# Performance work log

Hardware: AMD Instinct MI355X
Metric: run time of the kernel (lower is better)

The kernel has to match this reference:

```python
import jax, jax.numpy as jnp
import numpy as np

RADII = {1: 0.031, 2: 0.028, 3: 0.128, 4: 0.096, 5: 0.084, 6: 0.073, 7: 0.071, 8: 0.066, 9: 0.057, 10: 0.058, 11: 0.166, 12: 0.141, 13: 0.121, 14: 0.111, 15: 0.107, 16: 0.105, 17: 0.102, 18: 0.106, 19: 0.2029, 20: 0.176, 21: 0.17, 22: 0.16, 23: 0.153, 24: 0.139, 25: 0.15, 26: 0.142, 27: 0.138, 28: 0.124, 29: 0.132, 30: 0.122, 31: 0.122, 32: 0.12, 33: 0.119, 34: 0.12, 35: 0.12, 36: 0.116, 37: 0.22, 38: 0.195, 39: 0.19, 40: 0.175, 41: 0.164, 42: 0.154, 43: 0.147, 44: 0.146, 45: 0.142, 46: 0.139, 47: 0.145, 48: 0.144, 49: 0.142, 50: 0.139, 51: 0.139, 52: 0.138, 53: 0.139, 54: 0.14, 55: 0.244, 56: 0.215, 57: 0.207, 58: 0.204, 59: 0.2029, 60: 0.2009, 61: 0.199, 62: 0.198, 63: 0.198, 64: 0.196, 65: 0.194, 66: 0.192, 67: 0.192, 68: 0.189, 69: 0.19, 70: 0.187, 71: 0.187, 72: 0.175, 73: 0.17, 74: 0.162, 75: 0.151, 76: 0.144, 77: 0.141, 78: 0.136, 79: 0.136, 80: 0.132, 81: 0.145, 82: 0.146, 83: 0.148, 84: 0.14, 85: 0.15, 86: 0.15, 87: 0.26, 88: 0.221, 89: 0.215, 90: 0.206, 91: 0.2, 92: 0.196, 93: 0.19, 94: 0.187, 95: 0.18, 96: 0.169}

N_ATOMS = 1_000_000
N_EDGES = 16_000_000
NUM_SYSTEMS = 10_000
MAX_Z = 97  # atomic numbers 1..96 valid
COULOMB = 138.9354576   # kJ/mol * nm / e^2
A_PREF = 0.8854 * 0.0529177210903  # Bohr-radius prefactor in nm


def setup_inputs() -> dict:
    key = jax.random.key(0)
    k1, k2, k3, k4 = jax.random.split(key, 4)
    local_pair_indices = jax.random.randint(k1, (2, N_EDGES), 0, N_ATOMS)
    # positive distances in nm, safely away from zero
    local_d_ij = jax.random.uniform(k2, (N_EDGES,), jnp.float32, 0.01, 0.5)
    atomic_numbers = jax.random.randint(k3, (N_ATOMS,), 1, MAX_Z)
    atomic_subsystem_indices = jnp.sort(
        jax.random.randint(k4, (N_ATOMS,), 0, NUM_SYSTEMS))
    radii_table = np.zeros(MAX_Z, dtype=np.float32)
    for z, r in RADII.items():
        radii_table[z] = r
    return {
        'local_d_ij': local_d_ij,
        'radii_table': jnp.asarray(radii_table),
        'local_pair_indices': local_pair_indices,
        'atomic_numbers': atomic_numbers,
        'atomic_subsystem_indices': atomic_subsystem_indices,
    }


def reference(local_d_ij, radii_table, local_pair_indices, atomic_numbers,
              atomic_subsystem_indices):
    idx_i = local_pair_indices[0]
    idx_j = local_pair_indices[1]
    # torch filters edges by idx_i < idx_j (data-dependent shape); here we
    # keep fixed shapes and zero masked contributions -> identical sums.
    mask = idx_i < idx_j

    zi_int = atomic_numbers[idx_i]
    zj_int = atomic_numbers[idx_j]
    zi = zi_int.astype(jnp.float32)
    zj = zj_int.astype(jnp.float32)
    ri = radii_table[zi_int]
    rj = radii_table[zj_int]

    d_ij = local_d_ij
    a = A_PREF / (zi ** 0.23 + zj ** 0.23)
    d = d_ij / a
    f = (0.1818 * jnp.exp(-3.2 * d)
         + 0.5099 * jnp.exp(-0.9423 * d)
         + 0.2802 * jnp.exp(-0.4029 * d)
         + 0.02817 * jnp.exp(-0.2016 * d))
    rsum = ri + rj
    phi = jnp.where(d_ij < rsum,
                    0.5 * (jnp.cos(jnp.pi * d_ij / rsum) + 1.0),
                    0.0)
    energy = f * phi * COULOMB * zi * zj / d_ij
    energy = jnp.where(mask, energy, 0.0)

    seg = atomic_subsystem_indices[idx_i]
    per_system = jax.ops.segment_sum(energy, seg, num_segments=NUM_SYSTEMS)
    return per_system.reshape(-1, 1)
```

## Files before the change

### kernel.cpp

```cpp
#include <hip/hip_runtime.h>


constexpr int MAXZ = 97;
constexpr int NBINS_PAD = 10240;
constexpr int NREP = 512;
constexpr int NPART = 32;

constexpr double LOG2E_D = 1.4426950408889634;
constexpr float A_INV = (float)(1.0 / (0.8854 * 0.0529177210903));
constexpr float C1 = (float)(-3.2    * LOG2E_D);
constexpr float C2 = (float)(-0.9423 * LOG2E_D);
constexpr float C3 = (float)(-0.4029 * LOG2E_D);
constexpr float C4 = (float)(-0.2016 * LOG2E_D);
constexpr float COUL = 138.9354576f;

typedef int   iv4 __attribute__((ext_vector_type(4)));
typedef float fv4 __attribute__((ext_vector_type(4)));

__global__ void zero_kernel(float* __restrict__ out, int n) {
    int i = blockIdx.x * blockDim.x + threadIdx.x;
    if (i < n) out[i] = 0.0f;
}

__global__ void pack_kernel(const int* __restrict__ z,
                            const int* __restrict__ seg,
                            unsigned int* __restrict__ packed, int n) {
    int i = blockIdx.x * blockDim.x + threadIdx.x;
    if (i < n)
        packed[i] = (unsigned int)z[i] | ((unsigned int)seg[i] << 8);
}


__global__ __launch_bounds__(1024)
void zbl_hist_kernel(const float* __restrict__ d_ij,
                     const float* __restrict__ radii,
                     const int* __restrict__ idx_i,
                     const int* __restrict__ idx_j,
                     const unsigned int* __restrict__ packed,
                     float* __restrict__ rep,
                     int nchunk) {
    __shared__ float s_hist[NBINS_PAD];
    __shared__ float s_r[128];
    __shared__ float s_zp[128];
    const int t = threadIdx.x;

    for (int b = t; b < NBINS_PAD; b += 1024) s_hist[b] = 0.0f;
    if (t < 128) {
        s_r[t] = (t < MAXZ) ? radii[t] : 0.0f;
        s_zp[t] = __builtin_exp2f(0.23f * __builtin_log2f((float)t));
    }
    __syncthreads();

    const int stride = gridDim.x * blockDim.x;
    for (int c = blockIdx.x * blockDim.x + t; c < nchunk; c += stride) {
        iv4 ii = __builtin_nontemporal_load(
            reinterpret_cast<const iv4*>(idx_i) + c);
        iv4 jj = __builtin_nontemporal_load(
            reinterpret_cast<const iv4*>(idx_j) + c);
        fv4 dd = __builtin_nontemporal_load(
            reinterpret_cast<const fv4*>(d_ij) + c);

#pragma unroll
        for (int k = 0; k < 4; ++k) {
            int i = ii[k];
            int j = jj[k];
            float d = dd[k];
            if (i < j) {
                unsigned int pi = packed[i];
                unsigned int pj = packed[j];
                int zi = (int)(pi & 0xFFu);
                int zj = (int)(pj & 0xFFu);
                int seg = (int)(pi >> 8);
                float rsum = s_r[zi] + s_r[zj];
                if (d < rsum) {
                    float dA = d * (s_zp[zi] + s_zp[zj]) * A_INV;
                    float f = 0.1818f  * __builtin_exp2f(C1 * dA)
                            + 0.5099f  * __builtin_exp2f(C2 * dA)
                            + 0.2802f  * __builtin_exp2f(C3 * dA)
                            + 0.02817f * __builtin_exp2f(C4 * dA);
                    float tt = d * __builtin_amdgcn_rcpf(rsum);
                    float phi = 0.5f * (__builtin_amdgcn_cosf(0.5f * tt) + 1.0f);
                    float e = f * phi * (COUL * (float)zi * (float)zj)
                            * __builtin_amdgcn_rcpf(d);
                    atomicAdd(&s_hist[seg], e);
                }
            }
        }
    }

    __syncthreads();
    fv4* __restrict__ rp =
        reinterpret_cast<fv4*>(rep + (size_t)blockIdx.x * NBINS_PAD);
    const fv4* sh = reinterpret_cast<const fv4*>(s_hist);
    for (int q = t; q < NBINS_PAD / 4; q += 1024)
        __builtin_nontemporal_store(sh[q], rp + q);
}

__global__ __launch_bounds__(256)
void reduce1_kernel(const float* __restrict__ rep,
                    float* __restrict__ partial) {
    int bin = blockIdx.x * 256 + threadIdx.x;
    int s = blockIdx.y;
    float acc = 0.0f;
    for (int r = s; r < NREP; r += NPART)
        acc += rep[(size_t)r * NBINS_PAD + bin];
    partial[(size_t)s * NBINS_PAD + bin] = acc;
}

__global__ __launch_bounds__(256)
void reduce2_kernel(const float* __restrict__ partial,
                    float* __restrict__ out, int out_size) {
    int bin = blockIdx.x * 256 + threadIdx.x;
    if (bin < out_size) {
        float acc = 0.0f;
        for (int s = 0; s < NPART; ++s)
            acc += partial[(size_t)s * NBINS_PAD + bin];
        out[bin] = acc;
    }
}


template <bool PACKED>
__global__ __launch_bounds__(256)
void zbl_atomic_kernel(const float* __restrict__ d_ij,
                       const float* __restrict__ radii,
                       const int* __restrict__ idx_i,
                       const int* __restrict__ idx_j,
                       const unsigned int* __restrict__ packed,
                       const int* __restrict__ atomz,
                       const int* __restrict__ subsys,
                       float* __restrict__ out,
                       int nchunk) {
    __shared__ float s_r[128];
    __shared__ float s_zp[128];
    int t = threadIdx.x;
    if (t < 128) {
        s_r[t] = (t < MAXZ) ? radii[t] : 0.0f;
        s_zp[t] = __builtin_exp2f(0.23f * __builtin_log2f((float)t));
    }
    __syncthreads();

    int chunk = blockIdx.x * blockDim.x + threadIdx.x;
    if (chunk >= nchunk) return;

    iv4 ii = reinterpret_cast<const iv4*>(idx_i)[chunk];
    iv4 jj = reinterpret_cast<const iv4*>(idx_j)[chunk];
    fv4 dd = reinterpret_cast<const fv4*>(d_ij)[chunk];

#pragma unroll
    for (int k = 0; k < 4; ++k) {
        int i = ii[k];
        int j = jj[k];
        float d = dd[k];
        if (i < j) {
            int zi, zj, seg;
            if (PACKED) {
                unsigned int pi = packed[i];
                unsigned int pj = packed[j];
                zi = (int)(pi & 0xFFu);
                zj = (int)(pj & 0xFFu);
                seg = (int)(pi >> 8);
            } else {
                zi = atomz[i];
                zj = atomz[j];
                seg = subsys[i];
            }
            float rsum = s_r[zi] + s_r[zj];
            if (d < rsum) {
                float dA = d * (s_zp[zi] + s_zp[zj]) * A_INV;
                float f = 0.1818f  * __builtin_exp2f(C1 * dA)
                        + 0.5099f  * __builtin_exp2f(C2 * dA)
                        + 0.2802f  * __builtin_exp2f(C3 * dA)
                        + 0.02817f * __builtin_exp2f(C4 * dA);
                float tt = d * __builtin_amdgcn_rcpf(rsum);
                float phi = 0.5f * (__builtin_amdgcn_cosf(0.5f * tt) + 1.0f);
                float e = f * phi * (COUL * (float)zi * (float)zj)
                        * __builtin_amdgcn_rcpf(d);
                atomicAdd(out + seg, e);
            }
        }
    }
}

extern "C" void kernel_launch(void* const* d_in, const int* in_sizes, int n_in,
                              void* d_out, int out_size, void* d_ws, size_t ws_size,
                              hipStream_t stream) {
    const float* d_ij  = (const float*)d_in[0];
    const float* radii = (const float*)d_in[1];
    const int* pairs   = (const int*)d_in[2];
    const int* atomz   = (const int*)d_in[3];
    const int* subsys  = (const int*)d_in[4];
    float* out = (float*)d_out;

    const int n_edges = in_sizes[2] / 2;
    const int n_atoms = in_sizes[3];
    const int* idx_i = pairs;
    const int* idx_j = pairs + n_edges;
    const int nchunk = n_edges / 4;

    const size_t packed_bytes = (size_t)n_atoms * sizeof(unsigned int);
    const size_t rep_bytes = (size_t)NREP * NBINS_PAD * sizeof(float);
    const size_t part_bytes = (size_t)NPART * NBINS_PAD * sizeof(float);

    if (ws_size >= packed_bytes + rep_bytes + part_bytes) {
        unsigned int* packed = (unsigned int*)d_ws;
        float* rep = (float*)((char*)d_ws + packed_bytes);
        float* partial = (float*)((char*)d_ws + packed_bytes + rep_bytes);

        pack_kernel<<<(n_atoms + 255) / 256, 256, 0, stream>>>(atomz, subsys,
                                                               packed, n_atoms);
        zbl_hist_kernel<<<NREP, 1024, 0, stream>>>(
            d_ij, radii, idx_i, idx_j, packed, rep, nchunk);
        dim3 g1(NBINS_PAD / 256, NPART);
        reduce1_kernel<<<g1, 256, 0, stream>>>(rep, partial);
        reduce2_kernel<<<(out_size + 255) / 256, 256, 0, stream>>>(
            partial, out, out_size);
    } else {
        zero_kernel<<<(out_size + 255) / 256, 256, 0, stream>>>(out, out_size);
        const int blocks = (nchunk + 255) / 256;
        if (ws_size >= packed_bytes) {
            unsigned int* packed = (unsigned int*)d_ws;
            pack_kernel<<<(n_atoms + 255) / 256, 256, 0, stream>>>(
                atomz, subsys, packed, n_atoms);
            zbl_atomic_kernel<true><<<blocks, 256, 0, stream>>>(
                d_ij, radii, idx_i, idx_j, packed, atomz, subsys, out, nchunk);
        } else {
            zbl_atomic_kernel<false><<<blocks, 256, 0, stream>>>(
                d_ij, radii, idx_i, idx_j, nullptr, atomz, subsys, out, nchunk);
        }
    }
}
```

Measured before the change: 312.7 us.

## Compact masked edges into per-wave LDS queues before gathering and computing

The histogram kernel now loads one edge per lane and uses a wave ballot to compact the edges with i<j into a per-wave ring buffer in shared memory. It processes a full 64-edge batch only once the queue holds enough, so no lanes sit idle in the gather and transcendental work because of the mask. The cutoff branch is replaced by a select, and the radius and z^0.23 tables are merged into one float2 table. The histogram padding shrinks to 10016 bins. The cost is extra LDS traffic, scalar rather than vector edge loads, and work done for edges outside the cutoff.

```diff
diff --git a/kernel.cpp b/kernel.cpp
--- a/kernel.cpp
+++ b/kernel.cpp
@@ -2,9 +2,11 @@
 
 
 constexpr int MAXZ = 97;
-constexpr int NBINS_PAD = 10240;
+constexpr int NBINS_PAD = 10016;
 constexpr int NREP = 512;
 constexpr int NPART = 32;
+constexpr int WAVES_PER_BLOCK = 16;
+constexpr int QCAP = 128;
 
 constexpr double LOG2E_D = 1.4426950408889634;
 constexpr float A_INV = (float)(1.0 / (0.8854 * 0.0529177210903));
@@ -16,6 +18,7 @@
 
 typedef int   iv4 __attribute__((ext_vector_type(4)));
 typedef float fv4 __attribute__((ext_vector_type(4)));
+typedef float fv2 __attribute__((ext_vector_type(2)));
 
 __global__ void zero_kernel(float* __restrict__ out, int n) {
     int i = blockIdx.x * blockDim.x + threadIdx.x;
@@ -28,6 +31,32 @@
     int i = blockIdx.x * blockDim.x + threadIdx.x;
     if (i < n)
         packed[i] = (unsigned int)z[i] | ((unsigned int)seg[i] << 8);
+}
+
+__device__ __forceinline__ void process_edge(int i, int j, float d,
+                                             const unsigned int* __restrict__ packed,
+                                             const fv2* s_rz,
+                                             float* s_hist) {
+    unsigned int pi = packed[i];
+    unsigned int pj = packed[j];
+    int zi = (int)(pi & 0xFFu);
+    int zj = (int)(pj & 0xFFu);
+    int seg = (int)(pi >> 8);
+    fv2 rzi = s_rz[zi];
+    fv2 rzj = s_rz[zj];
+    float rsum = rzi.x + rzj.x;
+    bool ok = d < rsum;
+    float dA = d * (rzi.y + rzj.y) * A_INV;
+    float f = 0.1818f  * __builtin_exp2f(C1 * dA)
+            + 0.5099f  * __builtin_exp2f(C2 * dA)
+            + 0.2802f  * __builtin_exp2f(C3 * dA)
+            + 0.02817f * __builtin_exp2f(C4 * dA);
+    float tt = d * __builtin_amdgcn_rcpf(rsum);
+    float phi = 0.5f * (__builtin_amdgcn_cosf(0.5f * tt) + 1.0f);
+    float e = f * phi * (COUL * (float)zi * (float)zj)
+            * __builtin_amdgcn_rcpf(d);
+    e = ok ? e : 0.0f;
+    atomicAdd(&s_hist[seg], e);
 }
 
 
@@ -38,73 +67,91 @@
                      const int* __restrict__ idx_j,
                      const unsigned int* __restrict__ packed,
                      float* __restrict__ rep,
-                     int nchunk) {
+                     int n_edges) {
     __shared__ float s_hist[NBINS_PAD];
-    __shared__ float s_r[128];
-    __shared__ float s_zp[128];
+    __shared__ fv2   s_rz[100];
+    __shared__ int   s_qi[WAVES_PER_BLOCK * QCAP];
+    __shared__ int   s_qj[WAVES_PER_BLOCK * QCAP];
+    __shared__ float s_qd[WAVES_PER_BLOCK * QCAP];
     const int t = threadIdx.x;
+    const int lane = t & 63;
+    const int wave = t >> 6;
+    const int qbase = wave * QCAP;
 
     for (int b = t; b < NBINS_PAD; b += 1024) s_hist[b] = 0.0f;
-    if (t < 128) {
-        s_r[t] = (t < MAXZ) ? radii[t] : 0.0f;
-        s_zp[t] = __builtin_exp2f(0.23f * __builtin_log2f((float)t));
+    if (t < 100) {
+        fv2 v;
+        v.x = (t < MAXZ) ? radii[t] : 0.0f;
+        v.y = __builtin_exp2f(0.23f * __builtin_log2f((float)t));
+        s_rz[t] = v;
     }
     __syncthreads();
 
-    const int stride = gridDim.x * blockDim.x;
-    for (int c = blockIdx.x * blockDim.x + t; c < nchunk; c += stride) {
-        iv4 ii = __builtin_nontemporal_load(
-            reinterpret_cast<const iv4*>(idx_i) + c);
-        iv4 jj = __builtin_nontemporal_load(
-            reinterpret_cast<const iv4*>(idx_j) + c);
-        fv4 dd = __builtin_nontemporal_load(
-            reinterpret_cast<const fv4*>(d_ij) + c);
-
-#pragma unroll
-        for (int k = 0; k < 4; ++k) {
-            int i = ii[k];
-            int j = jj[k];
-            float d = dd[k];
-            if (i < j) {
-                unsigned int pi = packed[i];
-                unsigned int pj = packed[j];
-                int zi = (int)(pi & 0xFFu);
-                int zj = (int)(pj & 0xFFu);
-                int seg = (int)(pi >> 8);
-                float rsum = s_r[zi] + s_r[zj];
-                if (d < rsum) {
-                    float dA = d * (s_zp[zi] + s_zp[zj]) * A_INV;
-                    float f = 0.1818f  * __builtin_exp2f(C1 * dA)
-                            + 0.5099f  * __builtin_exp2f(C2 * dA)
-                            + 0.2802f  * __builtin_exp2f(C3 * dA)
-                            + 0.02817f * __builtin_exp2f(C4 * dA);
-                    float tt = d * __builtin_amdgcn_rcpf(rsum);
-                    float phi = 0.5f * (__builtin_amdgcn_cosf(0.5f * tt) + 1.0f);
-                    float e = f * phi * (COUL * (float)zi * (float)zj)
-                            * __builtin_amdgcn_rcpf(d);
-                    atomicAdd(&s_hist[seg], e);
-                }
-            }
-        }
+    const int nbatch = (n_edges + 63) >> 6;
+    const int wave_gid = (blockIdx.x << 4) + wave;
+    const int wstride = gridDim.x << 4;
+
+    int head = 0;
+    int q = 0;
+
+    for (int b = wave_gid; b < nbatch; b += wstride) {
+        int e = (b << 6) + lane;
+        bool inb = e < n_edges;
+        int eidx = inb ? e : 0;
+        int i = __builtin_nontemporal_load(idx_i + eidx);
+        int j = __builtin_nontemporal_load(idx_j + eidx);
+        float d = __builtin_nontemporal_load(d_ij + eidx);
+        bool m = inb && (i < j);
+
+        unsigned long long bal = __ballot(m);
+        int rank = __builtin_amdgcn_mbcnt_hi(
+            (unsigned int)(bal >> 32),
+            __builtin_amdgcn_mbcnt_lo((unsigned int)bal, 0));
+        int c = __popcll(bal);
+
+        if (m) {
+            int slot = qbase + ((head + q + rank) & (QCAP - 1));
+            s_qi[slot] = i;
+            s_qj[slot] = j;
+            s_qd[slot] = d;
+        }
+        q += c;
+
+        if (q >= 64) {
+            int slot = qbase + ((head + lane) & (QCAP - 1));
+            int qi = s_qi[slot];
+            int qj = s_qj[slot];
+            float qd = s_qd[slot];
+            head = (head + 64) & (QCAP - 1);
+            q -= 64;
+            process_edge(qi, qj, qd, packed, s_rz, s_hist);
+        }
+    }
+
+    if (lane < q) {
+        int slot = qbase + ((head + lane) & (QCAP - 1));
+        process_edge(s_qi[slot], s_qj[slot], s_qd[slot], packed, s_rz, s_hist);
     }
 
     __syncthreads();
     fv4* __restrict__ rp =
         reinterpret_cast<fv4*>(rep + (size_t)blockIdx.x * NBINS_PAD);
     const fv4* sh = reinterpret_cast<const fv4*>(s_hist);
-    for (int q = t; q < NBINS_PAD / 4; q += 1024)
-        __builtin_nontemporal_store(sh[q], rp + q);
+    for (int qv = t; qv < NBINS_PAD / 4; qv += 1024)
+        rp[qv] = sh[qv];
 }
 
 __global__ __launch_bounds__(256)
 void reduce1_kernel(const float* __restrict__ rep,
                     float* __restrict__ partial) {
     int bin = blockIdx.x * 256 + threadIdx.x;
-    int s = blockIdx.y;
-    float acc = 0.0f;
-    for (int r = s; r < NREP; r += NPART)
-        acc += rep[(size_t)r * NBINS_PAD + bin];
-    partial[(size_t)s * NBINS_PAD + bin] = acc;
+    if (bin < NBINS_PAD) {
+        int s = blockIdx.y;
+        float acc = 0.0f;
+        for (int r = s; r < NREP; r += NPART)
+            acc += rep[(size_t)r * NBINS_PAD + bin];
+        partial[(size_t)s * NBINS_PAD + bin] = acc;
+    }
 }
 
 __global__ __launch_bounds__(256)
@@ -131,12 +178,13 @@
                        const int* __restrict__ subsys,
                        float* __restrict__ out,
                        int nchunk) {
-    __shared__ float s_r[128];
-    __shared__ float s_zp[128];
+    __shared__ fv2 s_rz[100];
     int t = threadIdx.x;
-    if (t < 128) {
-        s_r[t] = (t < MAXZ) ? radii[t] : 0.0f;
-        s_zp[t] = __builtin_exp2f(0.23f * __builtin_log2f((float)t));
+    if (t < 100) {
+        fv2 v;
+        v.x = (t < MAXZ) ? radii[t] : 0.0f;
+        v.y = __builtin_exp2f(0.23f * __builtin_log2f((float)t));
+        s_rz[t] = v;
     }
     __syncthreads();
 
@@ -165,9 +213,10 @@
                 zj = atomz[j];
                 seg = subsys[i];
             }
-            float rsum = s_r[zi] + s_r[zj];
+            fv2 rzi = s_rz[zi], rzj = s_rz[zj];
+            float rsum = rzi.x + rzj.x;
             if (d < rsum) {
-                float dA = d * (s_zp[zi] + s_zp[zj]) * A_INV;
+                float dA = d * (rzi.y + rzj.y) * A_INV;
                 float f = 0.1818f  * __builtin_exp2f(C1 * dA)
                         + 0.5099f  * __builtin_exp2f(C2 * dA)
                         + 0.2802f  * __builtin_exp2f(C3 * dA)
@@ -196,7 +245,6 @@
     const int n_atoms = in_sizes[3];
     const int* idx_i = pairs;
     const int* idx_j = pairs + n_edges;
-    const int nchunk = n_edges / 4;
 
     const size_t packed_bytes = (size_t)n_atoms * sizeof(unsigned int);
     const size_t rep_bytes = (size_t)NREP * NBINS_PAD * sizeof(float);
@@ -210,13 +258,14 @@
         pack_kernel<<<(n_atoms + 255) / 256, 256, 0, stream>>>(atomz, subsys,
                                                                packed, n_atoms);
         zbl_hist_kernel<<<NREP, 1024, 0, stream>>>(
-            d_ij, radii, idx_i, idx_j, packed, rep, nchunk);
-        dim3 g1(NBINS_PAD / 256, NPART);
+            d_ij, radii, idx_i, idx_j, packed, rep, n_edges);
+        dim3 g1((NBINS_PAD + 255) / 256, NPART);
         reduce1_kernel<<<g1, 256, 0, stream>>>(rep, partial);
         reduce2_kernel<<<(out_size + 255) / 256, 256, 0, stream>>>(
             partial, out, out_size);
     } else {
         zero_kernel<<<(out_size + 255) / 256, 256, 0, stream>>>(out, out_size);
+        const int nchunk = n_edges / 4;
         const int blocks = (nchunk + 255) / 256;
         if (ws_size >= packed_bytes) {
             unsigned int* packed = (unsigned int*)d_ws;
```

Result: no change. 318.4 us (+1.8%).
